# Kernel optimization log

Hardware: AMD Instinct MI355X
Metric: run time of the kernel (lower is better)

## Reference

```python
import jax, jax.numpy as jnp
import numpy as np
from jax import lax

T, N, E, F, H, L, HL = 16, 10000, 320000, 128, 256, 64, 256


def setup_inputs() -> dict:
    key = jax.random.key(0)
    ks = iter(jax.random.split(key, 40))
    def nrm(shape, fan_in):
        return jax.random.normal(next(ks), shape, jnp.float32) * (1.0 / np.sqrt(fan_in))
    inp = {}
    inp["xs"] = jax.random.normal(next(ks), (T, N, F), jnp.float32)
    inp["edge_attr"] = jax.random.uniform(next(ks), (E,), jnp.float32)
    # encoder: GCN(F->H), GCN(H->H), Linear(H->L)
    inp["We0"], inp["be0"] = nrm((F, H), F), nrm((H,), H)
    inp["We1"], inp["be1"] = nrm((H, H), H), nrm((H,), H)
    inp["Wfce"], inp["bfce"] = nrm((H, L), H), nrm((L,), L)
    # 2-layer LSTM (torch gate order i,f,g,o; weights stored [in,4H])
    inp["Wih0"], inp["Whh0"] = nrm((L, 4 * HL), HL), nrm((HL, 4 * HL), HL)
    inp["bih0"], inp["bhh0"] = nrm((4 * HL,), HL), nrm((4 * HL,), HL)
    inp["Wih1"], inp["Whh1"] = nrm((HL, 4 * HL), HL), nrm((HL, 4 * HL), HL)
    inp["bih1"], inp["bhh1"] = nrm((4 * HL,), HL), nrm((4 * HL,), HL)
    inp["Whead"], inp["bhead"] = nrm((HL, L), HL), nrm((L,), L)
    # decoder: Linear(L -> N*L), GCN(L->H), GCN(H->H), GCN(H->F)
    inp["Wfcd"], inp["bfcd"] = nrm((L, N * L), L), nrm((N * L,), L)
    inp["Wd0"], inp["bd0"] = nrm((L, H), L), nrm((H,), H)
    inp["Wd1"], inp["bd1"] = nrm((H, H), H), nrm((H,), H)
    inp["Wd2"], inp["bd2"] = nrm((H, F), H), nrm((F,), F)
    inp["edge_index"] = jax.random.randint(next(ks), (2, E), 0, N, jnp.int64)
    return inp


def _forward(xs, edge_attr, We0, be0, We1, be1, Wfce, bfce,
             Wih0, Whh0, bih0, bhh0, Wih1, Whh1, bih1, bhh1,
             Whead, bhead, Wfcd, bfcd, Wd0, bd0, Wd1, bd1, Wd2, bd2,
             edge_index):
    n = xs.shape[1]
    loops = jnp.arange(n)
    src = jnp.concatenate([edge_index[0], loops])  # [E+N] with self-loops
    dst = jnp.concatenate([edge_index[1], loops])

    def gcn(x, ew, W, b):
        # PyG GCNConv: x@W then D^-1/2 A D^-1/2 scatter-add, + bias
        deg = jax.ops.segment_sum(ew, dst, num_segments=n)
        dis = jnp.where(deg > 0, lax.rsqrt(deg), 0.0)
        norm = dis[src] * ew * dis[dst]          # [E+N]
        h = x @ W                                # [N, Fout]
        return jax.ops.segment_sum(norm[:, None] * h[src], dst, num_segments=n) + b

    ew_enc = jnp.concatenate([edge_attr, jnp.ones((n,), edge_attr.dtype)])
    ew_dec = jnp.ones((src.shape[0],), xs.dtype)

    def encode(x):
        x = jax.nn.relu(gcn(x, ew_enc, We0, be0))
        x = jax.nn.relu(gcn(x, ew_enc, We1, be1))
        g = x.mean(axis=0)                       # global_mean_pool (single graph)
        return g @ Wfce + bfce                   # [L]

    zs = jax.vmap(encode)(xs)                    # [T, L]

    def lstm_layer(seq, Wih, Whh, bih, bhh):
        hdim = Whh.shape[0]
        def step(carry, xt):
            h, c = carry
            g = xt @ Wih + h @ Whh + bih + bhh
            i, f, gg, o = jnp.split(g, 4)
            c = jax.nn.sigmoid(f) * c + jax.nn.sigmoid(i) * jnp.tanh(gg)
            h = jax.nn.sigmoid(o) * jnp.tanh(c)
            return (h, c), h
        init = (jnp.zeros((hdim,), seq.dtype), jnp.zeros((hdim,), seq.dtype))
        return lax.scan(step, init, seq)[1]

    h1 = lstm_layer(zs, Wih0, Whh0, bih0, bhh0)
    h2 = lstm_layer(h1, Wih1, Whh1, bih1, bhh1)
    z = (h2 @ Whead + bhead)[-1]                 # last timestep, [L]

    x = jax.nn.relu(z @ Wfcd + bfcd).reshape(n, -1)  # [N, L]
    x = jax.nn.relu(gcn(x, ew_dec, Wd0, bd0))
    x = jax.nn.relu(gcn(x, ew_dec, Wd1, bd1))
    return gcn(x, ew_dec, Wd2, bd2)              # [N, F]


def reference(xs, edge_attr, We0, be0, We1, be1, Wfce, bfce,
              Wih0, Whh0, bih0, bhh0, Wih1, Whh1, bih1, bhh1,
              Whead, bhead, Wfcd, bfcd, Wd0, bd0, Wd1, bd1, Wd2, bd2,
              edge_index):
    return _forward(xs, edge_attr, We0, be0, We1, be1, Wfce, bfce,
                    Wih0, Whh0, bih0, bhh0, Wih1, Whh1, bih1, bhh1,
                    Whead, bhead, Wfcd, bfcd, Wd0, bd0, Wd1, bd1, Wd2, bd2,
                    edge_index)
```

## Files before the change

kernel.cpp:

```cpp
#include <hip/hip_runtime.h>
#include <math.h>

#define TT 16
#define NN 10000
#define EE 320000
#define FF 128
#define HH 256
#define LL 64
#define HLL 256

typedef _Float16 h16;
typedef _Float16 half4 __attribute__((ext_vector_type(4)));
typedef _Float16 half8 __attribute__((ext_vector_type(8)));
typedef float floatx4 __attribute__((ext_vector_type(4)));

__device__ __forceinline__ float sigm(float x) { return 1.0f / (1.0f + expf(-x)); }


__global__ void pre_deg(const int* __restrict__ src, const int* __restrict__ dst,
                        const float* __restrict__ ea, float* __restrict__ deg_enc,
                        int* __restrict__ cnt) {
    int e = blockIdx.x * 256 + threadIdx.x;
    if (e >= EE) return;
    int d = dst[e];
    atomicAdd(&deg_enc[d], ea[e]);
    atomicAdd(&cnt[d], 1);
}

__global__ void pre_dis(const float* __restrict__ deg_enc, const int* __restrict__ cnt,
                        float* __restrict__ dis_enc, float* __restrict__ dis_dec,
                        float* __restrict__ sn_enc, float* __restrict__ sn_dec) {
    int n = blockIdx.x * 256 + threadIdx.x;
    if (n >= NN) return;
    float de = deg_enc[n] + 1.0f;
    float dd = (float)cnt[n] + 1.0f;
    dis_enc[n] = rsqrtf(de);
    dis_dec[n] = rsqrtf(dd);
    sn_enc[n] = 1.0f / de;
    sn_dec[n] = 1.0f / dd;
}

__global__ void scan_rowptr(const int* __restrict__ cnt, int* __restrict__ row_ptr) {
    __shared__ int sb[1024];
    int tx = threadIdx.x;
    int run = 0;
    if (tx == 0) row_ptr[0] = 0;
    for (int base = 0; base < NN; base += 1024) {
        int i = base + tx;
        int v = (i < NN) ? cnt[i] : 0;
        sb[tx] = v;
        __syncthreads();
        for (int off = 1; off < 1024; off <<= 1) {
            int t = (tx >= off) ? sb[tx - off] : 0;
            __syncthreads();
            sb[tx] += t;
            __syncthreads();
        }
        if (i < NN) row_ptr[i + 1] = run + sb[tx];
        run += sb[1023];
        __syncthreads();
    }
}

__global__ void pre_build(const int* __restrict__ src, const int* __restrict__ dst,
                          const float* __restrict__ ea, const int* __restrict__ row_ptr,
                          int* __restrict__ cursor, const float* __restrict__ dis_enc,
                          const float* __restrict__ dis_dec, int* __restrict__ src_s,
                          float* __restrict__ w_enc, float* __restrict__ w_dec) {
    int e = blockIdx.x * 256 + threadIdx.x;
    if (e >= EE) return;
    int s = src[e], d = dst[e];
    int pos = row_ptr[d] + atomicAdd(&cursor[d], 1);
    src_s[pos] = s;
    w_enc[pos] = dis_enc[s] * ea[e] * dis_enc[d];
    w_dec[pos] = dis_dec[s] * dis_dec[d];
}


__global__ void cvt_f2h(const float* __restrict__ src, h16* __restrict__ dst, long n4) {
    long i = (long)blockIdx.x * 256 + threadIdx.x;
    if (i >= n4) return;
    float4 v = ((const float4*)src)[i];
    half4 o = {(h16)v.x, (h16)v.y, (h16)v.z, (h16)v.w};
    ((half4*)dst)[i] = o;
}

__global__ void wcvt(const float* __restrict__ Wsrc, h16* __restrict__ WT, int K, int N) {
    int i = blockIdx.x * 256 + threadIdx.x;
    if (i >= K * N) return;
    int n = i / K, k = i % K;
    WT[i] = (h16)Wsrc[(long)k * N + n];
}

template <int LPE, bool BIAS, bool RELU, bool OUT32>
__global__ __launch_bounds__(256) void spmm2(
    const h16* __restrict__ in, void* __restrict__ outv,
    const int* __restrict__ rp, const int* __restrict__ srcs,
    const float* __restrict__ w, const float* __restrict__ selfw,
    const float* __restrict__ bias, long sIn, long sOut, int tbatch) {
    constexpr int EPW = 64 / LPE;
    int g = blockIdx.x;
    int z, nb;
    if (tbatch > 1) {
        int gz = g & 7;
        int ph = g >> 3;
        nb = ph % (NN / 4);
        z = (ph / (NN / 4)) * 8 + gz;
    } else {
        z = 0;
        nb = g;
    }
    const half8* in8 = (const half8*)(in + (long)z * sIn);
    int wv = threadIdx.x >> 6;
    int node = nb * 4 + wv;
    int lane = threadIdx.x & 63;
    int c8 = lane & (LPE - 1);
    int el = lane / LPE;
    float acc[8] = {0.f, 0.f, 0.f, 0.f, 0.f, 0.f, 0.f, 0.f};
    if (el == 0) {
        half8 sv = in8[(long)node * LPE + c8];
        float sw = selfw[node];
#pragma unroll
        for (int i = 0; i < 8; ++i) acc[i] = sw * (float)sv[i];
    }
    int r1 = rp[node + 1];
    int j = rp[node] + el;
    for (; j + 3 * EPW < r1; j += 4 * EPW) {
        int s0 = srcs[j], s1 = srcs[j + EPW], s2 = srcs[j + 2 * EPW], s3 = srcs[j + 3 * EPW];
        float w0 = w[j], w1 = w[j + EPW], w2 = w[j + 2 * EPW], w3 = w[j + 3 * EPW];
        half8 v0 = in8[(long)s0 * LPE + c8];
        half8 v1 = in8[(long)s1 * LPE + c8];
        half8 v2 = in8[(long)s2 * LPE + c8];
        half8 v3 = in8[(long)s3 * LPE + c8];
#pragma unroll
        for (int i = 0; i < 8; ++i)
            acc[i] += w0 * (float)v0[i] + w1 * (float)v1[i] + w2 * (float)v2[i] + w3 * (float)v3[i];
    }
    for (; j < r1; j += EPW) {
        float wA = w[j];
        half8 vA = in8[(long)srcs[j] * LPE + c8];
#pragma unroll
        for (int i = 0; i < 8; ++i) acc[i] += wA * (float)vA[i];
    }
#pragma unroll
    for (int m = LPE; m < 64; m <<= 1) {
#pragma unroll
        for (int i = 0; i < 8; ++i) acc[i] += __shfl_xor(acc[i], m);
    }
    if (el == 0) {
        if (BIAS) {
            float4 b0 = *(const float4*)&bias[c8 * 8];
            float4 b1 = *(const float4*)&bias[c8 * 8 + 4];
            acc[0] += b0.x; acc[1] += b0.y; acc[2] += b0.z; acc[3] += b0.w;
            acc[4] += b1.x; acc[5] += b1.y; acc[6] += b1.z; acc[7] += b1.w;
        }
        if (RELU) {
#pragma unroll
            for (int i = 0; i < 8; ++i) acc[i] = fmaxf(acc[i], 0.f);
        }
        if (OUT32) {
            float* o = (float*)outv + (long)z * sOut + (long)node * (LPE * 8) + c8 * 8;
            *(float4*)o = make_float4(acc[0], acc[1], acc[2], acc[3]);
            *(float4*)(o + 4) = make_float4(acc[4], acc[5], acc[6], acc[7]);
        } else {
            half8 ov = {(h16)acc[0], (h16)acc[1], (h16)acc[2], (h16)acc[3],
                        (h16)acc[4], (h16)acc[5], (h16)acc[6], (h16)acc[7]};
            ((half8*)((h16*)outv + (long)z * sOut))[(long)node * LPE + c8] = ov;
        }
    }
}

template <bool BIAS, bool RELU>
__global__ __launch_bounds__(256) void gemm_h(
    const h16* __restrict__ A, const h16* __restrict__ BT,
    const float* __restrict__ bias, h16* __restrict__ C,
    int M, int Nc, int K, long sA, long sC) {
    A += (long)blockIdx.z * sA;
    C += (long)blockIdx.z * sC;
    __shared__ h16 smem[9216];
    h16* As = smem;
    h16* Bs = smem + 5120;
    int tid = threadIdx.x;
    int bm = blockIdx.y * 128, bn = blockIdx.x * 64;
    int w = tid >> 6, lane = tid & 63;
    int l15 = lane & 15, quad = lane >> 4;
    int ar = tid >> 2, ks = (tid & 3) * 8;
    floatx4 acc[2][4] = {};
    for (int k0 = 0; k0 < K; k0 += 32) {
        half8 a0 = {}, a1 = {};
        if (bm + ar < M) a0 = *(const half8*)&A[(long)(bm + ar) * K + k0 + ks];
        if (bm + ar + 64 < M) a1 = *(const half8*)&A[(long)(bm + ar + 64) * K + k0 + ks];
        *(half8*)&As[ar * 40 + ks] = a0;
        *(half8*)&As[(ar + 64) * 40 + ks] = a1;
        *(half8*)&Bs[ar * 40 + ks] = *(const half8*)&BT[(long)(bn + ar) * K + k0 + ks];
        __syncthreads();
        half8 af0 = *(const half8*)&As[(w * 32 + l15) * 40 + quad * 8];
        half8 af1 = *(const half8*)&As[(w * 32 + 16 + l15) * 40 + quad * 8];
#pragma unroll
        for (int nt = 0; nt < 4; ++nt) {
            half8 bf = *(const half8*)&Bs[(nt * 16 + l15) * 40 + quad * 8];
            acc[0][nt] = __builtin_amdgcn_mfma_f32_16x16x32_f16(af0, bf, acc[0][nt], 0, 0, 0);
            acc[1][nt] = __builtin_amdgcn_mfma_f32_16x16x32_f16(af1, bf, acc[1][nt], 0, 0, 0);
        }
        __syncthreads();
    }
    h16* Cs = smem;
#pragma unroll
    for (int nt = 0; nt < 4; ++nt) {
        float b = BIAS ? bias[bn + nt * 16 + l15] : 0.0f;
#pragma unroll
        for (int mf = 0; mf < 2; ++mf) {
#pragma unroll
            for (int r = 0; r < 4; ++r) {
                float v = acc[mf][nt][r] + b;
                if (RELU) v = fmaxf(v, 0.0f);
                Cs[(w * 32 + mf * 16 + quad * 4 + r) * 72 + nt * 16 + l15] = (h16)v;
            }
        }
    }
    __syncthreads();
#pragma unroll
    for (int p = 0; p < 2; ++p) {
        int r = (tid >> 2) + p * 64, sg = (tid & 3) * 16;
        if (bm + r < M) {
            half8 v0 = *(const half8*)&Cs[r * 72 + sg];
            half8 v1 = *(const half8*)&Cs[r * 72 + sg + 8];
            *(half8*)&C[(long)(bm + r) * Nc + bn + sg] = v0;
            *(half8*)&C[(long)(bm + r) * Nc + bn + sg + 8] = v1;
        }
    }
}

__global__ void col_mean_h(const h16* __restrict__ in, float* __restrict__ pooled, long sIn) {
    const h16* p = in + (long)blockIdx.z * sIn;
    float* pt = pooled + (long)blockIdx.z * HH;
    int c = threadIdx.x;
    int n0 = blockIdx.x * 64;
    int n1 = min(n0 + 64, NN);
    float acc = 0.f;
    for (int n = n0; n < n1; ++n) acc += (float)p[(long)n * HH + c];
    atomicAdd(&pt[c], acc * (1.0f / (float)NN));
}

__global__ void enc_head(const float* __restrict__ pooled, const float* __restrict__ Wfce,
                         const float* __restrict__ bfce, float* __restrict__ z) {
    int t = blockIdx.x, j = threadIdx.x;
    __shared__ float p[HH];
    for (int i = j; i < HH; i += 64) p[i] = pooled[t * HH + i];
    __syncthreads();
    float acc = bfce[j];
    for (int h = 0; h < HH; ++h) acc += p[h] * Wfce[h * LL + j];
    z[t * LL + j] = acc;
}

__global__ __launch_bounds__(256) void fused_lstm(
    const float* __restrict__ zenc,
    const float* __restrict__ Wih0, const float* __restrict__ Whh0,
    const float* __restrict__ bih0, const float* __restrict__ bhh0,
    const float* __restrict__ Wih1, const float* __restrict__ Whh1,
    const float* __restrict__ bih1, const float* __restrict__ bhh1,
    const float* __restrict__ Whead, const float* __restrict__ bhead,
    float* __restrict__ H1, float* __restrict__ H2,
    unsigned* __restrict__ bar, float* __restrict__ zdec) {
    __shared__ h16 Ws[256][64];
    __shared__ float Gs[16][64];
    __shared__ float part[4][64];
    __shared__ float hbuf[256];
    __shared__ float cbuf[16];
    int tid = threadIdx.x;
    int kq = tid >> 6;
    int col = tid & 63;
    int g4 = col >> 4, ul = col & 15;
    int u0 = blockIdx.x * 16;
    int jg = g4 * 256 + u0 + ul;
    unsigned gen = 0;

#define GBAR()                                                        \
    do {                                                              \
        __threadfence();                                              \
        __syncthreads();                                              \
        if (tid == 0) {                                               \
            ++gen;                                                    \
            atomicAdd(bar, 1u);                                       \
            while (atomicAdd(bar, 0u) < 16u * gen)                    \
                __builtin_amdgcn_s_sleep(2);                          \
        }                                                             \
        __syncthreads();                                              \
        __threadfence();                                              \
    } while (0)

    if (tid < 16) cbuf[tid] = 0.f;
    for (int idx = tid; idx < 256 * 64; idx += 256) {
        int k = idx >> 6, c = idx & 63;
        Ws[k][c] = (h16)Whh0[k * 1024 + (c >> 4) * 256 + u0 + (c & 15)];
    }
    {
        float b = bih0[jg] + bhh0[jg];
        float a0 = b, a1 = b, a2 = b, a3 = b;
        for (int k = 0; k < 64; ++k) {
            float wvv = Wih0[k * 1024 + jg];
            a0 += zenc[kq * 64 + k] * wvv;
            a1 += zenc[(kq + 4) * 64 + k] * wvv;
            a2 += zenc[(kq + 8) * 64 + k] * wvv;
            a3 += zenc[(kq + 12) * 64 + k] * wvv;
        }
        Gs[kq][col] = a0; Gs[kq + 4][col] = a1;
        Gs[kq + 8][col] = a2; Gs[kq + 12][col] = a3;
    }
    __syncthreads();
    for (int t = 1; t <= 16; ++t) {
        hbuf[tid] = H1[(t - 1) * 256 + tid];
        __syncthreads();
        float acc = 0.f;
#pragma unroll
        for (int i = 0; i < 64; ++i) acc += hbuf[kq * 64 + i] * (float)Ws[kq * 64 + i][col];
        part[kq][col] = acc;
        __syncthreads();
        if (tid < 16) {
            int u = tid;
            float i_ = Gs[t - 1][u]      + part[0][u]      + part[1][u]      + part[2][u]      + part[3][u];
            float f_ = Gs[t - 1][16 + u] + part[0][16 + u] + part[1][16 + u] + part[2][16 + u] + part[3][16 + u];
            float g_ = Gs[t - 1][32 + u] + part[0][32 + u] + part[1][32 + u] + part[2][32 + u] + part[3][32 + u];
            float o_ = Gs[t - 1][48 + u] + part[0][48 + u] + part[1][48 + u] + part[2][48 + u] + part[3][48 + u];
            float cc = sigm(f_) * cbuf[u] + sigm(i_) * tanhf(g_);
            cbuf[u] = cc;
            H1[t * 256 + u0 + u] = sigm(o_) * tanhf(cc);
        }
        GBAR();
    }
    if (tid < 16) cbuf[tid] = 0.f;
    for (int idx = tid; idx < 256 * 64; idx += 256) {
        int k = idx >> 6, c = idx & 63;
        Ws[k][c] = (h16)Whh1[k * 1024 + (c >> 4) * 256 + u0 + (c & 15)];
    }
    {
        float b = bih1[jg] + bhh1[jg];
        float a0 = b, a1 = b, a2 = b, a3 = b;
        for (int k = 0; k < 256; ++k) {
            float wvv = Wih1[k * 1024 + jg];
            a0 += H1[(kq + 1) * 256 + k] * wvv;
            a1 += H1[(kq + 5) * 256 + k] * wvv;
            a2 += H1[(kq + 9) * 256 + k] * wvv;
            a3 += H1[(kq + 13) * 256 + k] * wvv;
        }
        Gs[kq][col] = a0; Gs[kq + 4][col] = a1;
        Gs[kq + 8][col] = a2; Gs[kq + 12][col] = a3;
    }
    __syncthreads();
    for (int t = 1; t <= 16; ++t) {
        hbuf[tid] = H2[(t - 1) * 256 + tid];
        __syncthreads();
        float acc = 0.f;
#pragma unroll
        for (int i = 0; i < 64; ++i) acc += hbuf[kq * 64 + i] * (float)Ws[kq * 64 + i][col];
        part[kq][col] = acc;
        __syncthreads();
        if (tid < 16) {
            int u = tid;
            float i_ = Gs[t - 1][u]      + part[0][u]      + part[1][u]      + part[2][u]      + part[3][u];
            float f_ = Gs[t - 1][16 + u] + part[0][16 + u] + part[1][16 + u] + part[2][16 + u] + part[3][16 + u];
            float g_ = Gs[t - 1][32 + u] + part[0][32 + u] + part[1][32 + u] + part[2][32 + u] + part[3][32 + u];
            float o_ = Gs[t - 1][48 + u] + part[0][48 + u] + part[1][48 + u] + part[2][48 + u] + part[3][48 + u];
            float cc = sigm(f_) * cbuf[u] + sigm(i_) * tanhf(g_);
            cbuf[u] = cc;
            H2[t * 256 + u0 + u] = sigm(o_) * tanhf(cc);
        }
        GBAR();
    }
    if (blockIdx.x == 0 && tid < 64) {
        const float* hf = H2 + 16 * 256;
        float a = bhead[tid];
        for (int k = 0; k < 256; ++k) a += hf[k] * Whead[k * 64 + tid];
        zdec[tid] = a;
    }
#undef GBAR
}

__global__ void dec_fc(const float* __restrict__ z, const float* __restrict__ Wfcd,
                       const float* __restrict__ bfcd, h16* __restrict__ Xd) {
    __shared__ float zs_[LL];
    if (threadIdx.x < LL) zs_[threadIdx.x] = z[threadIdx.x];
    __syncthreads();
    long m = ((long)blockIdx.x * 256 + threadIdx.x) * 4;
    if (m >= (long)NN * LL) return;
    float4 acc = *(const float4*)&bfcd[m];
#pragma unroll
    for (int k = 0; k < LL; ++k) {
        float4 w4 = *(const float4*)&Wfcd[(long)k * (NN * (long)LL) + m];
        float zk = zs_[k];
        acc.x += zk * w4.x; acc.y += zk * w4.y; acc.z += zk * w4.z; acc.w += zk * w4.w;
    }
    half4 o = {(h16)fmaxf(acc.x, 0.f), (h16)fmaxf(acc.y, 0.f),
               (h16)fmaxf(acc.z, 0.f), (h16)fmaxf(acc.w, 0.f)};
    *(half4*)&Xd[m] = o;
}


extern "C" void kernel_launch(void* const* d_in, const int* in_sizes, int n_in,
                              void* d_out, int out_size, void* d_ws, size_t ws_size,
                              hipStream_t stream) {
    const float* xs = (const float*)d_in[0];
    const float* edge_attr = (const float*)d_in[1];
    const float* We0 = (const float*)d_in[2];  const float* be0 = (const float*)d_in[3];
    const float* We1 = (const float*)d_in[4];  const float* be1 = (const float*)d_in[5];
    const float* Wfce = (const float*)d_in[6]; const float* bfce = (const float*)d_in[7];
    const float* Wih0 = (const float*)d_in[8]; const float* Whh0 = (const float*)d_in[9];
    const float* bih0 = (const float*)d_in[10]; const float* bhh0 = (const float*)d_in[11];
    const float* Wih1 = (const float*)d_in[12]; const float* Whh1 = (const float*)d_in[13];
    const float* bih1 = (const float*)d_in[14]; const float* bhh1 = (const float*)d_in[15];
    const float* Whead = (const float*)d_in[16]; const float* bhead = (const float*)d_in[17];
    const float* Wfcd = (const float*)d_in[18]; const float* bfcd = (const float*)d_in[19];
    const float* Wd0 = (const float*)d_in[20]; const float* bd0 = (const float*)d_in[21];
    const float* Wd1 = (const float*)d_in[22]; const float* bd1 = (const float*)d_in[23];
    const float* Wd2 = (const float*)d_in[24]; const float* bd2 = (const float*)d_in[25];
    const int* eidx = (const int*)d_in[26];
    const int* esrc = eidx;
    const int* edst = eidx + EE;
    float* out = (float*)d_out;
    float* W = (float*)d_ws;

    const long O_DEG = 0;
    const long O_CNT = 10000;
    const long O_CUR = 20000;
    const long O_POOL = 30000;
    const long O_H1 = 34096;
    const long O_H2 = 38448;
    const long O_BAR = 42800;
    const long ZFLOATS = 42816;
    const long O_DISE = 42816, O_DISD = 52816, O_SNE = 62816, O_SND = 72816;
    const long O_RP = 82816;
    const long O_SRCS = 92832;
    const long O_WENC = 412832;
    const long O_WDEC = 732832;
    const long O_ZENC = 1052832;
    const long O_ZDEC = 1053856;
    const long O_F16 = 1053920;

    h16* Hbase = (h16*)(W + O_F16);
    const long HO_XS = 0;
    const long HO_WE0T = 20480000;
    const long HO_WE1T = HO_WE0T + 32768;
    const long HO_WD0T = HO_WE1T + 65536;
    const long HO_WD1T = HO_WD0T + 16384;
    const long HO_WD2T = HO_WD1T + 65536;
    const long HO_XD = HO_WD2T + 32768;
    const long HO_B0 = HO_XD + 640000;

    const long SB0 = (long)NN * FF;
    const long SB1 = (long)NN * HH;

    const long needBatched = O_F16 * 4 + (HO_B0 + 16L * (SB0 + 2 * SB1)) * 2;
    const bool batched = (long)ws_size >= needBatched;
    const long tb = batched ? 16 : 1;
    const long hoB1 = HO_B0 + tb * SB0;
    const long hoB2 = hoB1 + tb * SB1;

    float* deg = W + O_DEG;
    int* cnt = (int*)(W + O_CNT);
    int* cur = (int*)(W + O_CUR);
    float* pooled = W + O_POOL;
    float* H1 = W + O_H1; float* H2 = W + O_H2;
    unsigned* bar = (unsigned*)(W + O_BAR);
    float* dise = W + O_DISE; float* disd = W + O_DISD;
    float* sne = W + O_SNE;   float* snd = W + O_SND;
    int* rp = (int*)(W + O_RP);
    int* srcs = (int*)(W + O_SRCS);
    float* wenc = W + O_WENC; float* wdec = W + O_WDEC;
    float* zenc = W + O_ZENC; float* zdec = W + O_ZDEC;
    h16* xsh = Hbase + HO_XS;
    h16* We0T = Hbase + HO_WE0T; h16* We1T = Hbase + HO_WE1T;
    h16* Wd0T = Hbase + HO_WD0T; h16* Wd1T = Hbase + HO_WD1T; h16* Wd2T = Hbase + HO_WD2T;
    h16* XDh = Hbase + HO_XD;
    h16* B0h = Hbase + HO_B0; h16* B1h = Hbase + hoB1; h16* B2h = Hbase + hoB2;

    hipMemsetAsync(d_ws, 0, ZFLOATS * 4, stream);
    pre_deg<<<(EE + 255) / 256, 256, 0, stream>>>(esrc, edst, edge_attr, deg, cnt);
    pre_dis<<<(NN + 255) / 256, 256, 0, stream>>>(deg, cnt, dise, disd, sne, snd);
    scan_rowptr<<<1, 1024, 0, stream>>>(cnt, rp);
    pre_build<<<(EE + 255) / 256, 256, 0, stream>>>(esrc, edst, edge_attr, rp, cur, dise, disd,
                                                    srcs, wenc, wdec);
    cvt_f2h<<<20000, 256, 0, stream>>>(xs, xsh, (long)TT * NN * FF / 4);
    wcvt<<<(FF * HH + 255) / 256, 256, 0, stream>>>(We0, We0T, FF, HH);
    wcvt<<<(HH * HH + 255) / 256, 256, 0, stream>>>(We1, We1T, HH, HH);
    wcvt<<<(LL * HH + 255) / 256, 256, 0, stream>>>(Wd0, Wd0T, LL, HH);
    wcvt<<<(HH * HH + 255) / 256, 256, 0, stream>>>(Wd1, Wd1T, HH, HH);
    wcvt<<<(HH * FF + 255) / 256, 256, 0, stream>>>(Wd2, Wd2T, HH, FF);

    if (batched) {
        spmm2<16, false, false, false><<<dim3(2500 * 16), 256, 0, stream>>>(
            xsh, B0h, rp, srcs, wenc, sne, nullptr, SB0, SB0, 16);
        gemm_h<true, true><<<dim3(4, 79, 16), 256, 0, stream>>>(
            B0h, We0T, be0, B1h, NN, HH, FF, SB0, SB1);
        gemm_h<false, false><<<dim3(4, 79, 16), 256, 0, stream>>>(
            B1h, We1T, nullptr, B2h, NN, HH, HH, SB1, SB1);
        spmm2<32, true, true, false><<<dim3(2500 * 16), 256, 0, stream>>>(
            B2h, B1h, rp, srcs, wenc, sne, be1, SB1, SB1, 16);
        col_mean_h<<<dim3(157, 1, 16), 256, 0, stream>>>(B1h, pooled, SB1);
    } else {
        for (int t = 0; t < TT; ++t) {
            spmm2<16, false, false, false><<<dim3(2500), 256, 0, stream>>>(
                xsh + (long)t * SB0, B0h, rp, srcs, wenc, sne, nullptr, 0, 0, 1);
            gemm_h<true, true><<<dim3(4, 79, 1), 256, 0, stream>>>(
                B0h, We0T, be0, B1h, NN, HH, FF, 0, 0);
            gemm_h<false, false><<<dim3(4, 79, 1), 256, 0, stream>>>(
                B1h, We1T, nullptr, B2h, NN, HH, HH, 0, 0);
            spmm2<32, true, true, false><<<dim3(2500), 256, 0, stream>>>(
                B2h, B1h, rp, srcs, wenc, sne, be1, 0, 0, 1);
            col_mean_h<<<dim3(157, 1, 1), 256, 0, stream>>>(B1h, pooled + t * HH, 0);
        }
    }
    enc_head<<<16, 64, 0, stream>>>(pooled, Wfce, bfce, zenc);

    fused_lstm<<<16, 256, 0, stream>>>(zenc, Wih0, Whh0, bih0, bhh0,
                                       Wih1, Whh1, bih1, bhh1,
                                       Whead, bhead, H1, H2, bar, zdec);

    dec_fc<<<625, 256, 0, stream>>>(zdec, Wfcd, bfcd, XDh);
    spmm2<8, false, false, false><<<dim3(2500), 256, 0, stream>>>(
        XDh, B0h, rp, srcs, wdec, snd, nullptr, 0, 0, 1);
    gemm_h<true, true><<<dim3(4, 79, 1), 256, 0, stream>>>(
        B0h, Wd0T, bd0, B1h, NN, HH, LL, 0, 0);
    gemm_h<false, false><<<dim3(4, 79, 1), 256, 0, stream>>>(
        B1h, Wd1T, nullptr, B2h, NN, HH, HH, 0, 0);
    spmm2<32, true, true, false><<<dim3(2500), 256, 0, stream>>>(
        B2h, B1h, rp, srcs, wdec, snd, bd1, 0, 0, 1);
    gemm_h<false, false><<<dim3(2, 79, 1), 256, 0, stream>>>(
        B1h, Wd2T, nullptr, B0h, NN, FF, HH, 0, 0);
    spmm2<16, true, false, true><<<dim3(2500), 256, 0, stream>>>(
        B0h, out, rp, srcs, wdec, snd, bd2, 0, 0, 1);
}
```

Baseline: 1.094 ms.

## Pipeline both LSTM layers concurrently with per-timestep counters instead of global barriers

```diff
diff --git a/kernel.cpp b/kernel.cpp
--- a/kernel.cpp
+++ b/kernel.cpp
@@ -15,6 +15,16 @@
 typedef float floatx4 __attribute__((ext_vector_type(4)));
 
 __device__ __forceinline__ float sigm(float x) { return 1.0f / (1.0f + expf(-x)); }
+
+__device__ __forceinline__ float aldf(const float* p) {
+    return __hip_atomic_load(p, __ATOMIC_RELAXED, __HIP_MEMORY_SCOPE_AGENT);
+}
+__device__ __forceinline__ int aldi(const int* p) {
+    return __hip_atomic_load(p, __ATOMIC_RELAXED, __HIP_MEMORY_SCOPE_AGENT);
+}
+__device__ __forceinline__ void astf(float* p, float v) {
+    __hip_atomic_store(p, v, __ATOMIC_RELAXED, __HIP_MEMORY_SCOPE_AGENT);
+}
 
 
 __global__ void pre_deg(const int* __restrict__ src, const int* __restrict__ dst,
@@ -253,7 +263,7 @@
     z[t * LL + j] = acc;
 }
 
-__global__ __launch_bounds__(256) void fused_lstm(
+__global__ __launch_bounds__(256) void lstm_pipe(
     const float* __restrict__ zenc,
     const float* __restrict__ Wih0, const float* __restrict__ Whh0,
     const float* __restrict__ bih0, const float* __restrict__ bhh0,
@@ -261,119 +271,121 @@
     const float* __restrict__ bih1, const float* __restrict__ bhh1,
     const float* __restrict__ Whead, const float* __restrict__ bhead,
     float* __restrict__ H1, float* __restrict__ H2,
-    unsigned* __restrict__ bar, float* __restrict__ zdec) {
-    __shared__ h16 Ws[256][64];
-    __shared__ float Gs[16][64];
-    __shared__ float part[4][64];
-    __shared__ float hbuf[256];
+    int* __restrict__ cnt1, int* __restrict__ cnt2, float* __restrict__ zdec) {
+    __shared__ h16 Wr[256 * 64];
+    __shared__ h16 Wx[256 * 64];
+    __shared__ float Gs[16 * 64];
+    __shared__ float part[4 * 64];
+    __shared__ float hx[256];
+    __shared__ float hp[256];
     __shared__ float cbuf[16];
-    int tid = threadIdx.x;
-    int kq = tid >> 6;
-    int col = tid & 63;
+    int tid = threadIdx.x, kq = tid >> 6, col = tid & 63;
     int g4 = col >> 4, ul = col & 15;
-    int u0 = blockIdx.x * 16;
+    bool lay2 = blockIdx.x >= 16;
+    int ub = blockIdx.x & 15;
+    int u0 = ub * 16;
     int jg = g4 * 256 + u0 + ul;
-    unsigned gen = 0;
-
-#define GBAR()                                                        \
-    do {                                                              \
-        __threadfence();                                              \
-        __syncthreads();                                              \
-        if (tid == 0) {                                               \
-            ++gen;                                                    \
-            atomicAdd(bar, 1u);                                       \
-            while (atomicAdd(bar, 0u) < 16u * gen)                    \
-                __builtin_amdgcn_s_sleep(2);                          \
-        }                                                             \
-        __syncthreads();                                              \
-        __threadfence();                                              \
-    } while (0)
-
     if (tid < 16) cbuf[tid] = 0.f;
-    for (int idx = tid; idx < 256 * 64; idx += 256) {
-        int k = idx >> 6, c = idx & 63;
-        Ws[k][c] = (h16)Whh0[k * 1024 + (c >> 4) * 256 + u0 + (c & 15)];
-    }
-    {
-        float b = bih0[jg] + bhh0[jg];
-        float a0 = b, a1 = b, a2 = b, a3 = b;
-        for (int k = 0; k < 64; ++k) {
-            float wvv = Wih0[k * 1024 + jg];
-            a0 += zenc[kq * 64 + k] * wvv;
-            a1 += zenc[(kq + 4) * 64 + k] * wvv;
-            a2 += zenc[(kq + 8) * 64 + k] * wvv;
-            a3 += zenc[(kq + 12) * 64 + k] * wvv;
-        }
-        Gs[kq][col] = a0; Gs[kq + 4][col] = a1;
-        Gs[kq + 8][col] = a2; Gs[kq + 12][col] = a3;
-    }
-    __syncthreads();
-    for (int t = 1; t <= 16; ++t) {
-        hbuf[tid] = H1[(t - 1) * 256 + tid];
+
+    if (!lay2) {
+        for (int idx = tid; idx < 256 * 64; idx += 256) {
+            int k = idx >> 6, c = idx & 63;
+            Wr[idx] = (h16)Whh0[k * 1024 + (c >> 4) * 256 + u0 + (c & 15)];
+        }
+        {
+            float b = bih0[jg] + bhh0[jg];
+            float a0 = b, a1 = b, a2 = b, a3 = b;
+            for (int k = 0; k < 64; ++k) {
+                float wv = Wih0[k * 1024 + jg];
+                a0 += zenc[kq * 64 + k] * wv;
+                a1 += zenc[(kq + 4) * 64 + k] * wv;
+                a2 += zenc[(kq + 8) * 64 + k] * wv;
+                a3 += zenc[(kq + 12) * 64 + k] * wv;
+            }
+            Gs[kq * 64 + col] = a0; Gs[(kq + 4) * 64 + col] = a1;
+            Gs[(kq + 8) * 64 + col] = a2; Gs[(kq + 12) * 64 + col] = a3;
+        }
         __syncthreads();
-        float acc = 0.f;
-#pragma unroll
-        for (int i = 0; i < 64; ++i) acc += hbuf[kq * 64 + i] * (float)Ws[kq * 64 + i][col];
-        part[kq][col] = acc;
+        for (int t = 1; t <= 16; ++t) {
+            if (tid == 0 && t > 1)
+                while (aldi(&cnt1[t - 1]) < 16) __builtin_amdgcn_s_sleep(1);
+            __syncthreads();
+            hx[tid] = (t == 1) ? 0.f : aldf(&H1[(t - 1) * 256 + tid]);
+            __syncthreads();
+            float acc = 0.f;
+#pragma unroll
+            for (int i = 0; i < 64; ++i)
+                acc += hx[kq * 64 + i] * (float)Wr[(kq * 64 + i) * 64 + col];
+            part[kq * 64 + col] = acc;
+            __syncthreads();
+            if (tid < 16) {
+                int u = tid;
+                float i_ = Gs[(t - 1) * 64 + u]      + part[u]       + part[64 + u]       + part[128 + u]       + part[192 + u];
+                float f_ = Gs[(t - 1) * 64 + 16 + u] + part[16 + u]  + part[80 + u]       + part[144 + u]       + part[208 + u];
+                float g_ = Gs[(t - 1) * 64 + 32 + u] + part[32 + u]  + part[96 + u]       + part[160 + u]       + part[224 + u];
+                float o_ = Gs[(t - 1) * 64 + 48 + u] + part[48 + u]  + part[112 + u]      + part[176 + u]       + part[240 + u];
+                float cc = sigm(f_) * cbuf[u] + sigm(i_) * tanhf(g_);
+                cbuf[u] = cc;
+                astf(&H1[t * 256 + u0 + u], sigm(o_) * tanhf(cc));
+                __builtin_amdgcn_s_waitcnt(0);
+                if (tid == 0)
+                    __hip_atomic_fetch_add(&cnt1[t], 1, __ATOMIC_RELAXED, __HIP_MEMORY_SCOPE_AGENT);
+            }
+        }
+    } else {
+        for (int idx = tid; idx < 256 * 64; idx += 256) {
+            int k = idx >> 6, c = idx & 63;
+            int gcol = (c >> 4) * 256 + u0 + (c & 15);
+            Wr[idx] = (h16)Whh1[k * 1024 + gcol];
+            Wx[idx] = (h16)Wih1[k * 1024 + gcol];
+        }
+        float bj = bih1[jg] + bhh1[jg];
         __syncthreads();
-        if (tid < 16) {
-            int u = tid;
-            float i_ = Gs[t - 1][u]      + part[0][u]      + part[1][u]      + part[2][u]      + part[3][u];
-            float f_ = Gs[t - 1][16 + u] + part[0][16 + u] + part[1][16 + u] + part[2][16 + u] + part[3][16 + u];
-            float g_ = Gs[t - 1][32 + u] + part[0][32 + u] + part[1][32 + u] + part[2][32 + u] + part[3][32 + u];
-            float o_ = Gs[t - 1][48 + u] + part[0][48 + u] + part[1][48 + u] + part[2][48 + u] + part[3][48 + u];
-            float cc = sigm(f_) * cbuf[u] + sigm(i_) * tanhf(g_);
-            cbuf[u] = cc;
-            H1[t * 256 + u0 + u] = sigm(o_) * tanhf(cc);
-        }
-        GBAR();
-    }
-    if (tid < 16) cbuf[tid] = 0.f;
-    for (int idx = tid; idx < 256 * 64; idx += 256) {
-        int k = idx >> 6, c = idx & 63;
-        Ws[k][c] = (h16)Whh1[k * 1024 + (c >> 4) * 256 + u0 + (c & 15)];
-    }
-    {
-        float b = bih1[jg] + bhh1[jg];
-        float a0 = b, a1 = b, a2 = b, a3 = b;
-        for (int k = 0; k < 256; ++k) {
-            float wvv = Wih1[k * 1024 + jg];
-            a0 += H1[(kq + 1) * 256 + k] * wvv;
-            a1 += H1[(kq + 5) * 256 + k] * wvv;
-            a2 += H1[(kq + 9) * 256 + k] * wvv;
-            a3 += H1[(kq + 13) * 256 + k] * wvv;
-        }
-        Gs[kq][col] = a0; Gs[kq + 4][col] = a1;
-        Gs[kq + 8][col] = a2; Gs[kq + 12][col] = a3;
-    }
-    __syncthreads();
-    for (int t = 1; t <= 16; ++t) {
-        hbuf[tid] = H2[(t - 1) * 256 + tid];
-        __syncthreads();
-        float acc = 0.f;
-#pragma unroll
-        for (int i = 0; i < 64; ++i) acc += hbuf[kq * 64 + i] * (float)Ws[kq * 64 + i][col];
-        part[kq][col] = acc;
-        __syncthreads();
-        if (tid < 16) {
-            int u = tid;
-            float i_ = Gs[t - 1][u]      + part[0][u]      + part[1][u]      + part[2][u]      + part[3][u];
-            float f_ = Gs[t - 1][16 + u] + part[0][16 + u] + part[1][16 + u] + part[2][16 + u] + part[3][16 + u];
-            float g_ = Gs[t - 1][32 + u] + part[0][32 + u] + part[1][32 + u] + part[2][32 + u] + part[3][32 + u];
-            float o_ = Gs[t - 1][48 + u] + part[0][48 + u] + part[1][48 + u] + part[2][48 + u] + part[3][48 + u];
-            float cc = sigm(f_) * cbuf[u] + sigm(i_) * tanhf(g_);
-            cbuf[u] = cc;
-            H2[t * 256 + u0 + u] = sigm(o_) * tanhf(cc);
-        }
-        GBAR();
-    }
-    if (blockIdx.x == 0 && tid < 64) {
-        const float* hf = H2 + 16 * 256;
-        float a = bhead[tid];
-        for (int k = 0; k < 256; ++k) a += hf[k] * Whead[k * 64 + tid];
-        zdec[tid] = a;
-    }
-#undef GBAR
+        for (int t = 1; t <= 16; ++t) {
+            if (tid == 0) {
+                while (aldi(&cnt1[t]) < 16) __builtin_amdgcn_s_sleep(1);
+                if (t > 1)
+                    while (aldi(&cnt2[t - 1]) < 16) __builtin_amdgcn_s_sleep(1);
+            }
+            __syncthreads();
+            hx[tid] = aldf(&H1[t * 256 + tid]);
+            hp[tid] = (t == 1) ? 0.f : aldf(&H2[(t - 1) * 256 + tid]);
+            __syncthreads();
+            float acc = (kq == 0) ? bj : 0.f;
+#pragma unroll
+            for (int i = 0; i < 64; ++i) {
+                int k = kq * 64 + i;
+                acc += hx[k] * (float)Wx[k * 64 + col] + hp[k] * (float)Wr[k * 64 + col];
+            }
+            part[kq * 64 + col] = acc;
+            __syncthreads();
+            if (tid < 16) {
+                int u = tid;
+                float i_ = part[u]      + part[64 + u]  + part[128 + u] + part[192 + u];
+                float f_ = part[16 + u] + part[80 + u]  + part[144 + u] + part[208 + u];
+                float g_ = part[32 + u] + part[96 + u]  + part[160 + u] + part[224 + u];
+                float o_ = part[48 + u] + part[112 + u] + part[176 + u] + part[240 + u];
+                float cc = sigm(f_) * cbuf[u] + sigm(i_) * tanhf(g_);
+                cbuf[u] = cc;
+                astf(&H2[t * 256 + u0 + u], sigm(o_) * tanhf(cc));
+                __builtin_amdgcn_s_waitcnt(0);
+                if (tid == 0)
+                    __hip_atomic_fetch_add(&cnt2[t], 1, __ATOMIC_RELAXED, __HIP_MEMORY_SCOPE_AGENT);
+            }
+        }
+        if (ub == 0) {
+            if (tid == 0)
+                while (aldi(&cnt2[16]) < 16) __builtin_amdgcn_s_sleep(1);
+            __syncthreads();
+            hp[tid] = aldf(&H2[16 * 256 + tid]);
+            __syncthreads();
+            if (tid < 64) {
+                float a = bhead[tid];
+                for (int k = 0; k < 256; ++k) a += hp[k] * Whead[k * 64 + tid];
+                zdec[tid] = a;
+            }
+        }
+    }
 }
 
 __global__ void dec_fc(const float* __restrict__ z, const float* __restrict__ Wfcd,
@@ -425,16 +437,17 @@
     const long O_POOL = 30000;
     const long O_H1 = 34096;
     const long O_H2 = 38448;
-    const long O_BAR = 42800;
-    const long ZFLOATS = 42816;
-    const long O_DISE = 42816, O_DISD = 52816, O_SNE = 62816, O_SND = 72816;
-    const long O_RP = 82816;
-    const long O_SRCS = 92832;
-    const long O_WENC = 412832;
-    const long O_WDEC = 732832;
-    const long O_ZENC = 1052832;
-    const long O_ZDEC = 1053856;
-    const long O_F16 = 1053920;
+    const long O_CNT1 = 42800;
+    const long O_CNT2 = 42832;
+    const long ZFLOATS = 42864;
+    const long O_DISE = 42864, O_DISD = 52864, O_SNE = 62864, O_SND = 72864;
+    const long O_RP = 82864;
+    const long O_SRCS = 92880;
+    const long O_WENC = 412880;
+    const long O_WDEC = 732880;
+    const long O_ZENC = 1052880;
+    const long O_ZDEC = 1053904;
+    const long O_F16 = 1053968;
 
     h16* Hbase = (h16*)(W + O_F16);
     const long HO_XS = 0;
@@ -460,7 +473,7 @@
     int* cur = (int*)(W + O_CUR);
     float* pooled = W + O_POOL;
     float* H1 = W + O_H1; float* H2 = W + O_H2;
-    unsigned* bar = (unsigned*)(W + O_BAR);
+    int* cnt1 = (int*)(W + O_CNT1); int* cnt2 = (int*)(W + O_CNT2);
     float* dise = W + O_DISE; float* disd = W + O_DISD;
     float* sne = W + O_SNE;   float* snd = W + O_SND;
     int* rp = (int*)(W + O_RP);
@@ -511,9 +524,9 @@
     }
     enc_head<<<16, 64, 0, stream>>>(pooled, Wfce, bfce, zenc);
 
-    fused_lstm<<<16, 256, 0, stream>>>(zenc, Wih0, Whh0, bih0, bhh0,
-                                       Wih1, Whh1, bih1, bhh1,
-                                       Whead, bhead, H1, H2, bar, zdec);
+    lstm_pipe<<<32, 256, 0, stream>>>(zenc, Wih0, Whh0, bih0, bhh0,
+                                      Wih1, Whh1, bih1, bhh1,
+                                      Whead, bhead, H1, H2, cnt1, cnt2, zdec);
 
     dec_fc<<<625, 256, 0, stream>>>(zdec, Wfcd, bfcd, XDh);
     spmm2<8, false, false, false><<<dim3(2500), 256, 0, stream>>>(
```

New measurement: 1.009 ms. 1.08x faster.
